# Optimization experiments

Measured on AMD Instinct MI355X. Metric: run time of the kernel, lower is better.

## Reference

```python
import jax, jax.numpy as jnp
import numpy as np

M, K = 16384, 1024
G, N = 8, 2048


def setup_inputs() -> dict:
    key = jax.random.key(0)
    k1, k2, k3 = jax.random.split(key, 3)
    lhs = jax.random.normal(k1, (M, K), dtype=jnp.float32).astype(jnp.bfloat16)
    rhs = (jax.random.normal(k2, (G, N, K), dtype=jnp.float32) * 0.05).astype(jnp.bfloat16)
    m_indices = jax.random.randint(k3, (M,), 0, G, dtype=jnp.int32)
    return {"lhs": lhs, "rhs": rhs, "m_indices": m_indices}


def reference(lhs, rhs, m_indices):
    # Grouped GEMM: out[m, n] = sum_k lhs[m, k] * rhs[m_indices[m], n, k]
    # Kernel clamps out-of-range expert ids to 0, accumulates in fp32, emits bf16.
    g_count = rhs.shape[0]
    g = jnp.where((m_indices >= 0) & (m_indices < g_count), m_indices, 0)
    lhs_f = lhs.astype(jnp.float32)  # fp32 accumulation as in kernel
    acc = jnp.zeros((lhs.shape[0], rhs.shape[1]), dtype=jnp.float32)
    # Loop over small fixed expert count (G=8); each step is one dense GEMM,
    # rows are masked-selected per expert (no [M,N,K] gather materialized).
    for e in range(g_count):
        y = jnp.einsum('mk,nk->mn', lhs_f, rhs[e].astype(jnp.float32))  # [M, N]
        acc = jnp.where((g == e)[:, None], y, acc)
    return acc.astype(jnp.bfloat16)
```

## Files before the change

### kernel.cpp

```cpp
#include <hip/hip_runtime.h>
#include <hip/hip_bf16.h>

#define M_DIM 16384
#define K_DIM 1024
#define G_DIM 8
#define N_DIM 2048

#define BM 128
#define BN 128
#define BK 32
#define MT_PER_E 128

typedef short bf16x8 __attribute__((ext_vector_type(8)));
typedef float f32x4 __attribute__((ext_vector_type(4)));
typedef ushort us8 __attribute__((ext_vector_type(8)));

__device__ int g_bins[32];
__device__ int g_perm[M_DIM];

__global__ void zero_kernel() {
    if (threadIdx.x < 32) g_bins[threadIdx.x] = 0;
}

__global__ void hist_kernel(const int* __restrict__ mi) {
    int m = blockIdx.x * blockDim.x + threadIdx.x;
    if (m < M_DIM) {
        int g = mi[m];
        if (g < 0 || g >= G_DIM) g = 0;
        atomicAdd(&g_bins[g], 1);
    }
}

__global__ void scan_kernel() {
    if (threadIdx.x == 0 && blockIdx.x == 0) {
        int off = 0; g_bins[8] = 0;
        #pragma unroll
        for (int e = 0; e < G_DIM; ++e) { off += g_bins[e]; g_bins[9 + e] = off; }
        #pragma unroll
        for (int e = 0; e < G_DIM; ++e) g_bins[17 + e] = g_bins[8 + e];
    }
}

__global__ void scatter_kernel(const int* __restrict__ mi) {
    int m = blockIdx.x * blockDim.x + threadIdx.x;
    if (m < M_DIM) {
        int g = mi[m];
        if (g < 0 || g >= G_DIM) g = 0;
        int p = atomicAdd(&g_bins[17 + g], 1);
        g_perm[p] = m;
    }
}

__device__ __forceinline__ ushort f2b(float f) {
    return (ushort)(__float_as_uint(f) >> 16);
}

__device__ __forceinline__ us8 pack8(const float* p) {
    f32x4 u = *(const f32x4*)p;
    f32x4 v = *(const f32x4*)(p + 4);
    us8 o;
    o[0]=f2b(u[0]); o[1]=f2b(u[1]); o[2]=f2b(u[2]); o[3]=f2b(u[3]);
    o[4]=f2b(v[0]); o[5]=f2b(v[1]); o[6]=f2b(v[2]); o[7]=f2b(v[3]);
    return o;
}

__global__ __launch_bounds__(256) void gemm_kernel(
    const float* __restrict__ lhs,
    const float* __restrict__ rhs,
    float* __restrict__ out)
{
    const int e    = blockIdx.y >> 7;
    const int tile = blockIdx.y & 127;
    const int row_start = g_bins[8 + e] + tile * BM;
    const int row_end   = g_bins[9 + e];
    if (row_start >= row_end) return;
    const int valid = min(BM, row_end - row_start);
    const int bn = blockIdx.x * BN;

    __shared__ ushort lsA[BM * BK];
    __shared__ ushort lsB[BN * BK];
    __shared__ int prow[BM];

    const int t = threadIdx.x;
    if (t < BM) prow[t] = (t < valid) ? g_perm[row_start + t] : g_perm[row_start];
    __syncthreads();

    const int srow  = t >> 2;
    const int skoff = (t & 3) * 8;
    const float* a0 = lhs + (size_t)prow[srow] * K_DIM + skoff;
    const float* a1 = lhs + (size_t)prow[64 + srow] * K_DIM + skoff;
    const float* rhs_e = rhs + (size_t)e * N_DIM * K_DIM;
    const float* b0 = rhs_e + (size_t)(bn + srow) * K_DIM + skoff;
    const float* b1 = rhs_e + (size_t)(bn + 64 + srow) * K_DIM + skoff;

    const int lane = t & 63;
    const int wave = t >> 6;
    const int wr = wave >> 1;
    const int wc = wave & 1;
    const int lr = lane & 15;
    const int ko = (lane >> 4) * 8;

    f32x4 acc[4][4] = {};

    for (int k0 = 0; k0 < K_DIM; k0 += BK) {
        us8 pa0 = pack8(a0 + k0);
        us8 pa1 = pack8(a1 + k0);
        us8 pb0 = pack8(b0 + k0);
        us8 pb1 = pack8(b1 + k0);

        *(us8*)(lsA + t * 8)        = pa0;
        *(us8*)(lsA + 2048 + t * 8) = pa1;
        *(us8*)(lsB + t * 8)        = pb0;
        *(us8*)(lsB + 2048 + t * 8) = pb1;
        __syncthreads();

        bf16x8 af[4], bfr[4];
        #pragma unroll
        for (int m = 0; m < 4; ++m)
            af[m] = *(const bf16x8*)&lsA[(wr * 64 + m * 16 + lr) * BK + ko];
        #pragma unroll
        for (int n = 0; n < 4; ++n)
            bfr[n] = *(const bf16x8*)&lsB[(wc * 64 + n * 16 + lr) * BK + ko];

        #pragma unroll
        for (int m = 0; m < 4; ++m)
            #pragma unroll
            for (int n = 0; n < 4; ++n)
                acc[m][n] = __builtin_amdgcn_mfma_f32_16x16x32_bf16(
                    af[m], bfr[n], acc[m][n], 0, 0, 0);
        __syncthreads();
    }

    #pragma unroll
    for (int m = 0; m < 4; ++m) {
        #pragma unroll
        for (int j = 0; j < 4; ++j) {
            int lrow = wr * 64 + m * 16 + (lane >> 4) * 4 + j;
            if (lrow < valid) {
                size_t grow = (size_t)prow[lrow];
                #pragma unroll
                for (int n = 0; n < 4; ++n) {
                    int gcol = bn + wc * 64 + n * 16 + (lane & 15);
                    out[grow * N_DIM + gcol] = acc[m][n][j];
                }
            }
        }
    }
}

extern "C" void kernel_launch(void* const* d_in, const int* in_sizes, int n_in,
                              void* d_out, int out_size, void* d_ws, size_t ws_size,
                              hipStream_t stream) {
    const float* lhs = (const float*)d_in[0];
    const float* rhs = (const float*)d_in[1];
    const int* mi = (const int*)d_in[2];
    float* out = (float*)d_out;

    zero_kernel<<<1, 64, 0, stream>>>();
    hist_kernel<<<(M_DIM + 255) / 256, 256, 0, stream>>>(mi);
    scan_kernel<<<1, 64, 0, stream>>>();
    scatter_kernel<<<(M_DIM + 255) / 256, 256, 0, stream>>>(mi);

    dim3 grid(N_DIM / BN, G_DIM * MT_PER_E);
    gemm_kernel<<<grid, 256, 0, stream>>>(lhs, rhs, out);
}
```

Measured before the change: 264.9 us.

## Prefetch next K-tile into registers, swizzle LDS layout, pack bf16 with perm

```diff
diff --git a/kernel.cpp b/kernel.cpp
--- a/kernel.cpp
+++ b/kernel.cpp
@@ -13,7 +13,7 @@
 
 typedef short bf16x8 __attribute__((ext_vector_type(8)));
 typedef float f32x4 __attribute__((ext_vector_type(4)));
-typedef ushort us8 __attribute__((ext_vector_type(8)));
+typedef uint u32x4 __attribute__((ext_vector_type(4)));
 
 __device__ int g_bins[32];
 __device__ int g_perm[M_DIM];
@@ -51,16 +51,20 @@
     }
 }
 
-__device__ __forceinline__ ushort f2b(float f) {
-    return (ushort)(__float_as_uint(f) >> 16);
+__device__ __forceinline__ uint pkbf(float lo, float hi) {
+#if __has_builtin(__builtin_amdgcn_perm)
+    return __builtin_amdgcn_perm(__float_as_uint(hi), __float_as_uint(lo), 0x07060302u);
+#else
+    return (__float_as_uint(lo) >> 16) | (__float_as_uint(hi) & 0xffff0000u);
+#endif
 }
 
-__device__ __forceinline__ us8 pack8(const float* p) {
-    f32x4 u = *(const f32x4*)p;
-    f32x4 v = *(const f32x4*)(p + 4);
-    us8 o;
-    o[0]=f2b(u[0]); o[1]=f2b(u[1]); o[2]=f2b(u[2]); o[3]=f2b(u[3]);
-    o[4]=f2b(v[0]); o[5]=f2b(v[1]); o[6]=f2b(v[2]); o[7]=f2b(v[3]);
+__device__ __forceinline__ u32x4 pack8(f32x4 l, f32x4 h) {
+    u32x4 o;
+    o[0] = pkbf(l[0], l[1]);
+    o[1] = pkbf(l[2], l[3]);
+    o[2] = pkbf(h[0], h[1]);
+    o[3] = pkbf(h[2], h[3]);
     return o;
 }
 
@@ -93,43 +97,72 @@
     const float* b0 = rhs_e + (size_t)(bn + srow) * K_DIM + skoff;
     const float* b1 = rhs_e + (size_t)(bn + 64 + srow) * K_DIM + skoff;
 
+    const int wswz = (t * 16) ^ ((srow & 7) << 4);
+    char* const wA0 = (char*)lsA + wswz;
+    char* const wA1 = (char*)lsA + wswz + 4096;
+    char* const wB0 = (char*)lsB + wswz;
+    char* const wB1 = (char*)lsB + wswz + 4096;
+
     const int lane = t & 63;
     const int wave = t >> 6;
     const int wr = wave >> 1;
     const int wc = wave & 1;
     const int lr = lane & 15;
-    const int ko = (lane >> 4) * 8;
+    const int g16 = (lane >> 4) * 16;
+    const int rswz = (lr & 7) << 4;
 
     f32x4 acc[4][4] = {};
 
-    for (int k0 = 0; k0 < K_DIM; k0 += BK) {
-        us8 pa0 = pack8(a0 + k0);
-        us8 pa1 = pack8(a1 + k0);
-        us8 pb0 = pack8(b0 + k0);
-        us8 pb1 = pack8(b1 + k0);
+#define LOAD_STAGE(S, off) { \
+    S##a0l = *(const f32x4*)(a0 + (off)); S##a0h = *(const f32x4*)(a0 + (off) + 4); \
+    S##a1l = *(const f32x4*)(a1 + (off)); S##a1h = *(const f32x4*)(a1 + (off) + 4); \
+    S##b0l = *(const f32x4*)(b0 + (off)); S##b0h = *(const f32x4*)(b0 + (off) + 4); \
+    S##b1l = *(const f32x4*)(b1 + (off)); S##b1h = *(const f32x4*)(b1 + (off) + 4); }
 
-        *(us8*)(lsA + t * 8)        = pa0;
-        *(us8*)(lsA + 2048 + t * 8) = pa1;
-        *(us8*)(lsB + t * 8)        = pb0;
-        *(us8*)(lsB + 2048 + t * 8) = pb1;
-        __syncthreads();
+#define COMMIT_STAGE(S) { \
+    *(u32x4*)wA0 = pack8(S##a0l, S##a0h); \
+    *(u32x4*)wA1 = pack8(S##a1l, S##a1h); \
+    *(u32x4*)wB0 = pack8(S##b0l, S##b0h); \
+    *(u32x4*)wB1 = pack8(S##b1l, S##b1h); \
+    __syncthreads(); \
+    bf16x8 af0 = *(const bf16x8*)((const char*)lsA + (((wr*64 +  0 + lr)*64 + g16) ^ rswz)); \
+    bf16x8 af1 = *(const bf16x8*)((const char*)lsA + (((wr*64 + 16 + lr)*64 + g16) ^ rswz)); \
+    bf16x8 af2 = *(const bf16x8*)((const char*)lsA + (((wr*64 + 32 + lr)*64 + g16) ^ rswz)); \
+    bf16x8 af3 = *(const bf16x8*)((const char*)lsA + (((wr*64 + 48 + lr)*64 + g16) ^ rswz)); \
+    bf16x8 bf0 = *(const bf16x8*)((const char*)lsB + (((wc*64 +  0 + lr)*64 + g16) ^ rswz)); \
+    bf16x8 bf1 = *(const bf16x8*)((const char*)lsB + (((wc*64 + 16 + lr)*64 + g16) ^ rswz)); \
+    bf16x8 bf2 = *(const bf16x8*)((const char*)lsB + (((wc*64 + 32 + lr)*64 + g16) ^ rswz)); \
+    bf16x8 bf3 = *(const bf16x8*)((const char*)lsB + (((wc*64 + 48 + lr)*64 + g16) ^ rswz)); \
+    acc[0][0] = __builtin_amdgcn_mfma_f32_16x16x32_bf16(af0, bf0, acc[0][0], 0,0,0); \
+    acc[0][1] = __builtin_amdgcn_mfma_f32_16x16x32_bf16(af0, bf1, acc[0][1], 0,0,0); \
+    acc[0][2] = __builtin_amdgcn_mfma_f32_16x16x32_bf16(af0, bf2, acc[0][2], 0,0,0); \
+    acc[0][3] = __builtin_amdgcn_mfma_f32_16x16x32_bf16(af0, bf3, acc[0][3], 0,0,0); \
+    acc[1][0] = __builtin_amdgcn_mfma_f32_16x16x32_bf16(af1, bf0, acc[1][0], 0,0,0); \
+    acc[1][1] = __builtin_amdgcn_mfma_f32_16x16x32_bf16(af1, bf1, acc[1][1], 0,0,0); \
+    acc[1][2] = __builtin_amdgcn_mfma_f32_16x16x32_bf16(af1, bf2, acc[1][2], 0,0,0); \
+    acc[1][3] = __builtin_amdgcn_mfma_f32_16x16x32_bf16(af1, bf3, acc[1][3], 0,0,0); \
+    acc[2][0] = __builtin_amdgcn_mfma_f32_16x16x32_bf16(af2, bf0, acc[2][0], 0,0,0); \
+    acc[2][1] = __builtin_amdgcn_mfma_f32_16x16x32_bf16(af2, bf1, acc[2][1], 0,0,0); \
+    acc[2][2] = __builtin_amdgcn_mfma_f32_16x16x32_bf16(af2, bf2, acc[2][2], 0,0,0); \
+    acc[2][3] = __builtin_amdgcn_mfma_f32_16x16x32_bf16(af2, bf3, acc[2][3], 0,0,0); \
+    acc[3][0] = __builtin_amdgcn_mfma_f32_16x16x32_bf16(af3, bf0, acc[3][0], 0,0,0); \
+    acc[3][1] = __builtin_amdgcn_mfma_f32_16x16x32_bf16(af3, bf1, acc[3][1], 0,0,0); \
+    acc[3][2] = __builtin_amdgcn_mfma_f32_16x16x32_bf16(af3, bf2, acc[3][2], 0,0,0); \
+    acc[3][3] = __builtin_amdgcn_mfma_f32_16x16x32_bf16(af3, bf3, acc[3][3], 0,0,0); \
+    __syncthreads(); }
 
-        bf16x8 af[4], bfr[4];
-        #pragma unroll
-        for (int m = 0; m < 4; ++m)
-            af[m] = *(const bf16x8*)&lsA[(wr * 64 + m * 16 + lr) * BK + ko];
-        #pragma unroll
-        for (int n = 0; n < 4; ++n)
-            bfr[n] = *(const bf16x8*)&lsB[(wc * 64 + n * 16 + lr) * BK + ko];
+    f32x4 Xa0l,Xa0h,Xa1l,Xa1h,Xb0l,Xb0h,Xb1l,Xb1h;
+    f32x4 Ya0l,Ya0h,Ya1l,Ya1h,Yb0l,Yb0h,Yb1l,Yb1h;
 
-        #pragma unroll
-        for (int m = 0; m < 4; ++m)
-            #pragma unroll
-            for (int n = 0; n < 4; ++n)
-                acc[m][n] = __builtin_amdgcn_mfma_f32_16x16x32_bf16(
-                    af[m], bfr[n], acc[m][n], 0, 0, 0);
-        __syncthreads();
+    LOAD_STAGE(X, 0)
+    for (int k0 = 0; k0 < K_DIM; k0 += 2 * BK) {
+        LOAD_STAGE(Y, k0 + BK)
+        COMMIT_STAGE(X)
+        if (k0 + 2 * BK < K_DIM) LOAD_STAGE(X, k0 + 2 * BK)
+        COMMIT_STAGE(Y)
     }
+#undef LOAD_STAGE
+#undef COMMIT_STAGE
 
     #pragma unroll
     for (int m = 0; m < 4; ++m) {
```

New measurement: 265.9 us. No clear change (+0.4%).

## Pre-convert fp32 inputs to bf16 in workspace and load tiles via global_load_lds

Applied to the files above, without the earlier changes.

```diff
diff --git a/kernel.cpp b/kernel.cpp
--- a/kernel.cpp
+++ b/kernel.cpp
@@ -11,9 +11,13 @@
 #define BK 32
 #define MT_PER_E 128
 
+#define WS_NEEDED (2ull * 16777216ull * 2ull)
+
 typedef short bf16x8 __attribute__((ext_vector_type(8)));
 typedef float f32x4 __attribute__((ext_vector_type(4)));
+typedef ushort us4 __attribute__((ext_vector_type(4)));
 typedef ushort us8 __attribute__((ext_vector_type(8)));
+typedef uint u32x4 __attribute__((ext_vector_type(4)));
 
 __device__ int g_bins[32];
 __device__ int g_perm[M_DIM];
@@ -55,18 +59,27 @@
     return (ushort)(__float_as_uint(f) >> 16);
 }
 
-__device__ __forceinline__ us8 pack8(const float* p) {
-    f32x4 u = *(const f32x4*)p;
-    f32x4 v = *(const f32x4*)(p + 4);
-    us8 o;
-    o[0]=f2b(u[0]); o[1]=f2b(u[1]); o[2]=f2b(u[2]); o[3]=f2b(u[3]);
-    o[4]=f2b(v[0]); o[5]=f2b(v[1]); o[6]=f2b(v[2]); o[7]=f2b(v[3]);
-    return o;
-}
-
-__global__ __launch_bounds__(256) void gemm_kernel(
-    const float* __restrict__ lhs,
-    const float* __restrict__ rhs,
+__global__ __launch_bounds__(256) void pack_kernel(
+    const float* __restrict__ src, ushort* __restrict__ dst, int n4)
+{
+    int i = blockIdx.x * blockDim.x + threadIdx.x;
+    for (; i < n4; i += gridDim.x * blockDim.x) {
+        f32x4 v = ((const f32x4*)src)[i];
+        us4 o;
+        o[0] = f2b(v[0]); o[1] = f2b(v[1]); o[2] = f2b(v[2]); o[3] = f2b(v[3]);
+        ((us4*)dst)[i] = o;
+    }
+}
+
+__device__ __forceinline__ void gload_lds16(const ushort* g, ushort* l) {
+    __builtin_amdgcn_global_load_lds(
+        (const __attribute__((address_space(1))) void*)g,
+        (__attribute__((address_space(3))) void*)l, 16, 0, 0);
+}
+
+__global__ __launch_bounds__(256) void gemm_ws_kernel(
+    const ushort* __restrict__ lhs,
+    const ushort* __restrict__ rhs,
     float* __restrict__ out)
 {
     const int e    = blockIdx.y >> 7;
@@ -87,11 +100,15 @@
 
     const int srow  = t >> 2;
     const int skoff = (t & 3) * 8;
-    const float* a0 = lhs + (size_t)prow[srow] * K_DIM + skoff;
-    const float* a1 = lhs + (size_t)prow[64 + srow] * K_DIM + skoff;
-    const float* rhs_e = rhs + (size_t)e * N_DIM * K_DIM;
-    const float* b0 = rhs_e + (size_t)(bn + srow) * K_DIM + skoff;
-    const float* b1 = rhs_e + (size_t)(bn + 64 + srow) * K_DIM + skoff;
+    const ushort* a0 = lhs + (size_t)prow[srow] * K_DIM + skoff;
+    const ushort* a1 = lhs + (size_t)prow[64 + srow] * K_DIM + skoff;
+    const ushort* rhs_e = rhs + (size_t)e * N_DIM * K_DIM;
+    const ushort* b0 = rhs_e + (size_t)(bn + srow) * K_DIM + skoff;
+    const ushort* b1 = rhs_e + (size_t)(bn + 64 + srow) * K_DIM + skoff;
+    ushort* dA0 = lsA + t * 8;
+    ushort* dA1 = lsA + 2048 + t * 8;
+    ushort* dB0 = lsB + t * 8;
+    ushort* dB1 = lsB + 2048 + t * 8;
 
     const int lane = t & 63;
     const int wave = t >> 6;
@@ -103,15 +120,10 @@
     f32x4 acc[4][4] = {};
 
     for (int k0 = 0; k0 < K_DIM; k0 += BK) {
-        us8 pa0 = pack8(a0 + k0);
-        us8 pa1 = pack8(a1 + k0);
-        us8 pb0 = pack8(b0 + k0);
-        us8 pb1 = pack8(b1 + k0);
-
-        *(us8*)(lsA + t * 8)        = pa0;
-        *(us8*)(lsA + 2048 + t * 8) = pa1;
-        *(us8*)(lsB + t * 8)        = pb0;
-        *(us8*)(lsB + 2048 + t * 8) = pb1;
+        gload_lds16(a0 + k0, dA0);
+        gload_lds16(a1 + k0, dA1);
+        gload_lds16(b0 + k0, dB0);
+        gload_lds16(b1 + k0, dB1);
         __syncthreads();
 
         bf16x8 af[4], bfr[4];
@@ -148,6 +160,93 @@
     }
 }
 
+__device__ __forceinline__ us8 pack8(const float* p) {
+    f32x4 u = *(const f32x4*)p;
+    f32x4 v = *(const f32x4*)(p + 4);
+    us8 o;
+    o[0]=f2b(u[0]); o[1]=f2b(u[1]); o[2]=f2b(u[2]); o[3]=f2b(u[3]);
+    o[4]=f2b(v[0]); o[5]=f2b(v[1]); o[6]=f2b(v[2]); o[7]=f2b(v[3]);
+    return o;
+}
+
+__global__ __launch_bounds__(256) void gemm_f32_kernel(
+    const float* __restrict__ lhs, const float* __restrict__ rhs,
+    float* __restrict__ out)
+{
+    const int e    = blockIdx.y >> 7;
+    const int tile = blockIdx.y & 127;
+    const int row_start = g_bins[8 + e] + tile * BM;
+    const int row_end   = g_bins[9 + e];
+    if (row_start >= row_end) return;
+    const int valid = min(BM, row_end - row_start);
+    const int bn = blockIdx.x * BN;
+
+    __shared__ ushort lsA[BM * BK];
+    __shared__ ushort lsB[BN * BK];
+    __shared__ int prow[BM];
+
+    const int t = threadIdx.x;
+    if (t < BM) prow[t] = (t < valid) ? g_perm[row_start + t] : g_perm[row_start];
+    __syncthreads();
+
+    const int srow  = t >> 2;
+    const int skoff = (t & 3) * 8;
+    const float* a0 = lhs + (size_t)prow[srow] * K_DIM + skoff;
+    const float* a1 = lhs + (size_t)prow[64 + srow] * K_DIM + skoff;
+    const float* rhs_e = rhs + (size_t)e * N_DIM * K_DIM;
+    const float* b0 = rhs_e + (size_t)(bn + srow) * K_DIM + skoff;
+    const float* b1 = rhs_e + (size_t)(bn + 64 + srow) * K_DIM + skoff;
+
+    const int lane = t & 63;
+    const int wave = t >> 6;
+    const int wr = wave >> 1;
+    const int wc = wave & 1;
+    const int lr = lane & 15;
+    const int ko = (lane >> 4) * 8;
+
+    f32x4 acc[4][4] = {};
+
+    for (int k0 = 0; k0 < K_DIM; k0 += BK) {
+        *(us8*)(lsA + t * 8)        = pack8(a0 + k0);
+        *(us8*)(lsA + 2048 + t * 8) = pack8(a1 + k0);
+        *(us8*)(lsB + t * 8)        = pack8(b0 + k0);
+        *(us8*)(lsB + 2048 + t * 8) = pack8(b1 + k0);
+        __syncthreads();
+
+        bf16x8 af[4], bfr[4];
+        #pragma unroll
+        for (int m = 0; m < 4; ++m)
+            af[m] = *(const bf16x8*)&lsA[(wr * 64 + m * 16 + lr) * BK + ko];
+        #pragma unroll
+        for (int n = 0; n < 4; ++n)
+            bfr[n] = *(const bf16x8*)&lsB[(wc * 64 + n * 16 + lr) * BK + ko];
+
+        #pragma unroll
+        for (int m = 0; m < 4; ++m)
+            #pragma unroll
+            for (int n = 0; n < 4; ++n)
+                acc[m][n] = __builtin_amdgcn_mfma_f32_16x16x32_bf16(
+                    af[m], bfr[n], acc[m][n], 0, 0, 0);
+        __syncthreads();
+    }
+
+    #pragma unroll
+    for (int m = 0; m < 4; ++m) {
+        #pragma unroll
+        for (int j = 0; j < 4; ++j) {
+            int lrow = wr * 64 + m * 16 + (lane >> 4) * 4 + j;
+            if (lrow < valid) {
+                size_t grow = (size_t)prow[lrow];
+                #pragma unroll
+                for (int n = 0; n < 4; ++n) {
+                    int gcol = bn + wc * 64 + n * 16 + (lane & 15);
+                    out[grow * N_DIM + gcol] = acc[m][n][j];
+                }
+            }
+        }
+    }
+}
+
 extern "C" void kernel_launch(void* const* d_in, const int* in_sizes, int n_in,
                               void* d_out, int out_size, void* d_ws, size_t ws_size,
                               hipStream_t stream) {
@@ -162,5 +261,15 @@
     scatter_kernel<<<(M_DIM + 255) / 256, 256, 0, stream>>>(mi);
 
     dim3 grid(N_DIM / BN, G_DIM * MT_PER_E);
-    gemm_kernel<<<grid, 256, 0, stream>>>(lhs, rhs, out);
-}
+
+    if (ws_size >= WS_NEEDED) {
+        ushort* wsA = (ushort*)d_ws;
+        ushort* wsB = wsA + (size_t)M_DIM * K_DIM;
+        const int n4 = (M_DIM * K_DIM) / 4;
+        pack_kernel<<<2048, 256, 0, stream>>>(lhs, wsA, n4);
+        pack_kernel<<<2048, 256, 0, stream>>>(rhs, wsB, n4);
+        gemm_ws_kernel<<<grid, 256, 0, stream>>>(wsA, wsB, out);
+    } else {
+        gemm_f32_kernel<<<grid, 256, 0, stream>>>(lhs, rhs, out);
+    }
+}
```

After: 287.8 us. +8.6%, slower.
